# Kernel optimization log

Hardware: AMD Instinct MI355X
Metric: run time of the kernel (lower is better)

The kernel has to match this reference:

```python
import jax, jax.numpy as jnp
import numpy as np

B, H, W, C = 1, 64, 64, 768
NUM_HEADS = 12
HEAD_DIM = C // NUM_HEADS  # 64


def setup_inputs() -> dict:
    key = jax.random.key(0)
    ks = jax.random.split(key, 7)
    s = 0.02
    return {
        "imagelike_bhwc": jax.random.normal(ks[0], (B, H, W, C), dtype=jnp.float32),
        "qkv_w": jax.random.normal(ks[1], (C, 3 * C), dtype=jnp.float32) * s,
        "qkv_b": jax.random.normal(ks[2], (3 * C,), dtype=jnp.float32) * s,
        "proj_w": jax.random.normal(ks[3], (C, C), dtype=jnp.float32) * s,
        "proj_b": jax.random.normal(ks[4], (C,), dtype=jnp.float32) * s,
        "rel_pos_h": jax.random.normal(ks[5], (2 * H - 1, HEAD_DIM), dtype=jnp.float32) * s,
        "rel_pos_w": jax.random.normal(ks[6], (2 * W - 1, HEAD_DIM), dtype=jnp.float32) * s,
    }


def reference(imagelike_bhwc, qkv_w, qkv_b, proj_w, proj_b, rel_pos_h, rel_pos_w):
    b, h, w, c = imagelike_bhwc.shape
    n = h * w
    nh, hd = NUM_HEADS, c // NUM_HEADS
    scale = hd ** (-0.5)

    # qkv projection -> (3, B*nh, N, hd)
    qkv = imagelike_bhwc @ qkv_w + qkv_b  # (b,h,w,3c)
    qkv = qkv.reshape(b, n, 3, nh, hd).transpose(2, 0, 3, 1, 4).reshape(3, b * nh, n, hd)
    q, k, v = qkv[0], qkv[1], qkv[2]

    # scaled dot-product scores
    attn = jnp.einsum("bqd,bkd->bqk", q * scale, k)  # (b*nh, n, n)

    # decomposed relative position bias (query grid == key grid == base grid)
    idx_h = jnp.arange(h)[:, None] - jnp.arange(h)[None, :] + (h - 1)  # (h,h)
    idx_w = jnp.arange(w)[:, None] - jnp.arange(w)[None, :] + (w - 1)  # (w,w)
    Rh = rel_pos_h[idx_h]  # (h, h, hd)
    Rw = rel_pos_w[idx_w]  # (w, w, hd)
    r_q = q.reshape(b * nh, h, w, hd)
    rel_h = jnp.einsum("bhwc,hkc->bhwk", r_q, Rh)  # (b*nh, h, w, h)
    rel_w = jnp.einsum("bhwc,wkc->bhwk", r_q, Rw)  # (b*nh, h, w, w)
    bias = (rel_h[:, :, :, :, None] + rel_w[:, :, :, None, :]).reshape(b * nh, n, n)

    attn = jax.nn.softmax(attn + bias, axis=-1)
    out = jnp.einsum("bqk,bkd->bqd", attn, v)  # (b*nh, n, hd)

    out = out.reshape(b, nh, h, w, hd).transpose(0, 2, 3, 1, 4).reshape(b, h, w, c)
    return out @ proj_w + proj_b
```

## Files before the change

kernel.cpp:

```cpp
#include <hip/hip_runtime.h>
#include <stdint.h>

typedef unsigned short u16;
typedef __bf16 bf16x8 __attribute__((ext_vector_type(8)));
typedef float f32x4 __attribute__((ext_vector_type(4)));
typedef unsigned short ushort8 __attribute__((ext_vector_type(8)));
typedef unsigned short ushort4v __attribute__((ext_vector_type(4)));
typedef uint32_t uint4v __attribute__((ext_vector_type(4)));

#define MFMA __builtin_amdgcn_mfma_f32_16x16x32_bf16
#define EXP2 __builtin_amdgcn_exp2f

__device__ __forceinline__ u16 f2bf(float f){
  uint32_t u = __builtin_bit_cast(uint32_t, f);
  u += 0x7fffu + ((u >> 16) & 1u);
  return (u16)(u >> 16);
}
__device__ __forceinline__ float bf2f(u16 h){
  uint32_t u = ((uint32_t)h) << 16;
  return __builtin_bit_cast(float, u);
}
__device__ __forceinline__ uint32_t cvtpk(float lo, float hi){
  uint32_t r;
  asm("v_cvt_pk_bf16_f32 %0, %1, %2" : "=v"(r) : "v"(lo), "v"(hi));
  return r;
}
__device__ __forceinline__ bf16x8 ld8(const u16* p){
  return __builtin_bit_cast(bf16x8, *(const ushort8*)p);
}
__device__ __forceinline__ void gload16(const void* g, void* l){
  __builtin_amdgcn_global_load_lds((__attribute__((address_space(1))) void*)(void*)g,
                                   (__attribute__((address_space(3))) void*)l, 16, 0, 0);
}


__device__ __forceinline__ void tr_body(const float* __restrict__ in, u16* __restrict__ out,
                                        int R, int Cc, int bx, int by, int t, float* tile ){
  int r0 = bx*64, c0 = by*64;
  int c = t & 63, r4 = t >> 6;
  for (int i = 0; i < 16; ++i)
    tile[(r4 + i*4)*65 + c] = in[(size_t)(r0 + r4 + i*4)*Cc + c0 + c];
  __syncthreads();
  for (int i = 0; i < 16; ++i){
    int rr = r4 + i*4;
    out[(size_t)(c0 + rr)*R + r0 + c] = f2bf(tile[c*65 + rr]);
  }
}

__global__ __launch_bounds__(256) void k_prep(const float* __restrict__ X32,
                                              const float* __restrict__ qkvw,
                                              const float* __restrict__ projw,
                                              const float* __restrict__ rposh,
                                              const float* __restrict__ rposw,
                                              u16* __restrict__ Xb, u16* __restrict__ W1T,
                                              u16* __restrict__ PT,
                                              u16* __restrict__ rh8, u16* __restrict__ rw8){
  __shared__ float tile[64*65];
  const int b = blockIdx.x, t = threadIdx.x;
  if (b < 1536){
    int i = b*256 + t;
    const float4* p = (const float4*)X32;
    float4 a = p[i*2], c = p[i*2+1];
    ushort8 o;
    o[0]=f2bf(a.x); o[1]=f2bf(a.y); o[2]=f2bf(a.z); o[3]=f2bf(a.w);
    o[4]=f2bf(c.x); o[5]=f2bf(c.y); o[6]=f2bf(c.z); o[7]=f2bf(c.w);
    ((ushort8*)Xb)[i] = o;
  } else if (b < 1968){
    int bb = b - 1536;
    tr_body(qkvw, W1T, 768, 2304, bb % 12, bb / 12, t, tile);
  } else if (b < 2112){
    int bb = b - 1968;
    tr_body(projw, PT, 768, 768, bb % 12, bb / 12, t, tile);
  } else {
    int i = (b - 2112)*256 + t;
    if (i < 8192)      rh8[i] = f2bf(i < 8128 ? rposh[i]*8.0f : 0.0f);
    else { int j = i - 8192; rw8[j] = f2bf(j < 8128 ? rposw[j]*8.0f : 0.0f); }
  }
}


__global__ __launch_bounds__(256) void k_qkv(const u16* __restrict__ X, const u16* __restrict__ WT,
                                             const float* __restrict__ bias,
                                             u16* __restrict__ Qs, u16* __restrict__ Kf, u16* __restrict__ Vf){
  __shared__ __align__(16) u16 At[128*64];
  __shared__ __align__(16) u16 Bt[128*64];
  __shared__ __align__(16) u16 Tt[4][64*72];
  const int tid = threadIdx.x, lane = tid & 63, w = tid >> 6;
  const int m0 = blockIdx.x*128, n0 = blockIdx.y*128;
  const int wr = (w >> 1)*64, wc = (w & 1)*64;
  const int lr = lane & 15, lg = lane >> 4;
  const int srcRow = w*32 + (lane >> 3);
  const int srcK   = (lane & 7)*8;
  f32x4 acc[4][4] = {};
  for (int kt = 0; kt < 12; ++kt){
    const int kbase = kt*64;
    for (int s = 0; s < 4; ++s){
      gload16(X  + (size_t)(m0 + srcRow + s*8)*768 + kbase + srcK, At + (w*32 + s*8)*64);
      gload16(WT + (size_t)(n0 + srcRow + s*8)*768 + kbase + srcK, Bt + (w*32 + s*8)*64);
    }
    __syncthreads();
    bf16x8 af[2][4], bfr[2][4];
    for (int ks = 0; ks < 2; ++ks)
      for (int i = 0; i < 4; ++i){
        af[ks][i]  = ld8(At + (wr + i*16 + lr)*64 + ks*32 + lg*8);
        bfr[ks][i] = ld8(Bt + (wc + i*16 + lr)*64 + ks*32 + lg*8);
      }
    for (int ks = 0; ks < 2; ++ks)
      for (int mi = 0; mi < 4; ++mi)
        for (int ni = 0; ni < 4; ++ni)
          acc[mi][ni] = MFMA(af[ks][mi], bfr[ks][ni], acc[mi][ni], 0, 0, 0);
    __syncthreads();
  }
  const int colbase = n0 + wc;
  const int s3 = colbase / 768;
  const int hh = (colbase % 768) >> 6;
  const int rowbase = m0 + wr;
  if (s3 == 0){
    for (int mi = 0; mi < 4; ++mi)
      for (int ni = 0; ni < 4; ++ni){
        float bv = bias[colbase + ni*16 + lr];
        for (int r = 0; r < 4; ++r){
          int row = rowbase + mi*16 + lg*4 + r;
          Qs[((size_t)hh*4096 + row)*64 + ni*16 + lr] =
              f2bf((acc[mi][ni][r] + bv)*(0.125f*1.44269504f));
        }
      }
  } else {
    u16* T = Tt[w];
    for (int mi = 0; mi < 4; ++mi)
      for (int ni = 0; ni < 4; ++ni){
        float bv = bias[colbase + ni*16 + lr];
        for (int r = 0; r < 4; ++r){
          int row_l = mi*16 + lg*4 + r, col_l = ni*16 + lr;
          u16 v = f2bf(acc[mi][ni][r] + bv);
          if (s3 == 1) T[row_l*72 + col_l] = v;
          else         T[col_l*72 + row_l] = v;
        }
      }
    const int kb = rowbase >> 6;
    u16* dst = (s3 == 1 ? Kf : Vf) + ((size_t)hh*64 + kb)*4096 + lane*8;
    if (s3 == 1){
      #pragma unroll
      for (int f = 0; f < 8; ++f){
        int a = f >> 1, ks = f & 1;
        *(ushort8*)&dst[f*512] = *(const ushort8*)&T[(a*16 + lr)*72 + ks*32 + lg*8];
      }
    } else {
      #pragma unroll
      for (int f = 0; f < 8; ++f){
        int a = f >> 1, ks = f & 1;
        const int rowb = (a*16 + lr)*72 + ks*32 + lg*4;
        ushort4v lo = *(const ushort4v*)&T[rowb];
        ushort4v hi = *(const ushort4v*)&T[rowb + 16];
        ushort8 o;
        o[0]=lo[0]; o[1]=lo[1]; o[2]=lo[2]; o[3]=lo[3];
        o[4]=hi[0]; o[5]=hi[1]; o[6]=hi[2]; o[7]=hi[3];
        *(ushort8*)&dst[f*512] = o;
      }
    }
  }
}


__global__ __launch_bounds__(256) void k_rel(const u16* __restrict__ Qs, const u16* __restrict__ Rh8,
                                             const u16* __restrict__ Rw8,
                                             u16* __restrict__ relh, u16* __restrict__ relw){
  __shared__ __align__(16) u16 Ql[64*64];
  __shared__ __align__(16) u16 Rhl[64*64];
  __shared__ __align__(16) u16 Rwl[128*64];
  const int tid = threadIdx.x, lane = tid & 63, w = tid >> 6;
  const int qh = blockIdx.x, h = blockIdx.y;
  const int lr = lane & 15, lg = lane >> 4;
  for (int j = 0; j < 2; ++j){
    int ch = tid + 256*j;
    int row = ch >> 3, k8 = (ch & 7)*8;
    *(ushort8*)&Ql[row*64 + k8]  = *(const ushort8*)&Qs[((size_t)h*4096 + qh*64 + row)*64 + k8];
    *(ushort8*)&Rhl[row*64 + k8] = *(const ushort8*)&Rh8[(qh + row)*64 + k8];
  }
  for (int j = 0; j < 4; ++j){
    int ch = tid + 256*j;
    int row = ch >> 3, k8 = (ch & 7)*8;
    *(ushort8*)&Rwl[row*64 + k8] = *(const ushort8*)&Rw8[row*64 + k8];
  }
  __syncthreads();
  bf16x8 a[2];
  for (int ks = 0; ks < 2; ++ks) a[ks] = ld8(Ql + (w*16 + lr)*64 + ks*32 + lg*8);
  for (int ct = 0; ct < 4; ++ct){
    f32x4 c = {};
    for (int ks = 0; ks < 2; ++ks)
      c = MFMA(a[ks], ld8(Rhl + (ct*16 + lr)*64 + ks*32 + lg*8), c, 0, 0, 0);
    int kh = 63 - (ct*16 + lr);
    for (int r = 0; r < 4; ++r){
      int qw = w*16 + lg*4 + r;
      relh[((size_t)h*4096 + qh*64 + qw)*64 + kh] = f2bf(c[r]);
    }
  }
  for (int ct = 0; ct < 8; ++ct){
    f32x4 c = {};
    for (int ks = 0; ks < 2; ++ks)
      c = MFMA(a[ks], ld8(Rwl + (ct*16 + lr)*64 + ks*32 + lg*8), c, 0, 0, 0);
    int cc = ct*16 + lr;
    for (int r = 0; r < 4; ++r){
      int qw = w*16 + lg*4 + r;
      int kw = qw + 63 - cc;
      if (kw >= 0 && kw < 64)
        relw[((size_t)h*4096 + qh*64 + qw)*64 + kw] = f2bf(c[r]);
    }
  }
}


__global__ __launch_bounds__(256, 3) void k_flash(const u16* __restrict__ Qs, const u16* __restrict__ Kf,
                                                  const u16* __restrict__ Vf,
                                                  const u16* __restrict__ relh, const u16* __restrict__ relw,
                                                  u16* __restrict__ Ob){
  __shared__ __align__(16) u16 Kl[2][4096];
  __shared__ __align__(16) u16 Vl[2][4096];
  const int tid = threadIdx.x, lane = tid & 63, w = tid >> 6;
  const int b = blockIdx.x;
  const int p = (b & 7)*96 + (b >> 3);
  const int h = p >> 6, qb = p & 63;
  const int lr = lane & 15, lg = lane >> 4;
  const size_t hq = (size_t)h*4096;
  const int q = qb*64 + w*16 + lr;

  const bf16x8 qf0 = ld8(Qs + (hq + q)*64 + lg*8);
  const bf16x8 qf1 = ld8(Qs + (hq + q)*64 + 32 + lg*8);
  float rwf[4][4];
  #pragma unroll
  for (int ct = 0; ct < 4; ++ct){
    ushort4v t = *(const ushort4v*)&relw[(hq + q)*64 + ct*16 + lg*4];
    #pragma unroll
    for (int r = 0; r < 4; ++r) rwf[ct][r] = bf2f(t[r]);
  }

  const u16* KfH = Kf + (size_t)h*262144;
  const u16* VfH = Vf + (size_t)h*262144;
  const u16* rhbase = relh + (hq + q)*64;

  float m = -1e30f, lsum = 0.f;
  f32x4 oacc[4] = {};

  auto stage = [&](int buf, int kb){
    const u16* ks = KfH + kb*4096 + w*1024 + lane*8;
    const u16* vs = VfH + kb*4096 + w*1024 + lane*8;
    gload16(ks,       &Kl[buf][w*1024]);
    gload16(ks + 512, &Kl[buf][w*1024 + 512]);
    gload16(vs,       &Vl[buf][w*1024]);
    gload16(vs + 512, &Vl[buf][w*1024 + 512]);
  };

#define ITERBODY(KB, BUF)                                                     \
  {                                                                           \
    const u16* KL = Kl[BUF] + lane*8;                                         \
    const u16* VL = Vl[BUF] + lane*8;                                         \
    const float rhv = bf2f(rhbase[KB]);                                       \
    f32x4 s[4];                                                               \
    _Pragma("unroll")                                                         \
    for (int ct = 0; ct < 4; ++ct){                                           \
      _Pragma("unroll")                                                       \
      for (int r = 0; r < 4; ++r) s[ct][r] = rhv + rwf[ct][r];                \
    }                                                                         \
    __builtin_amdgcn_s_setprio(1);                                            \
    _Pragma("unroll")                                                         \
    for (int ct = 0; ct < 4; ++ct){                                           \
      s[ct] = MFMA(ld8(KL + (ct*2)*512),   qf0, s[ct], 0, 0, 0);              \
      s[ct] = MFMA(ld8(KL + (ct*2+1)*512), qf1, s[ct], 0, 0, 0);              \
    }                                                                         \
    __builtin_amdgcn_s_setprio(0);                                            \
                                       \
    float pm0 = fmaxf(fmaxf(s[0][0], s[0][1]), fmaxf(fmaxf(s[0][2], s[0][3]), \
                      fmaxf(s[1][0], s[1][1])));                              \
    float pm1 = fmaxf(fmaxf(s[1][2], s[1][3]), fmaxf(fmaxf(s[2][0], s[2][1]), \
                      fmaxf(s[2][2], s[2][3])));                              \
    float pm2 = fmaxf(fmaxf(s[3][0], s[3][1]), fmaxf(s[3][2], s[3][3]));      \
    float pm = fmaxf(fmaxf(pm0, pm1), pm2);                                   \
             \
    if (__any(pm > m)){                                                       \
      pm = fmaxf(pm, __shfl_xor(pm, 16, 64));                                 \
      pm = fmaxf(pm, __shfl_xor(pm, 32, 64));                                 \
      const float nm = fmaxf(m, pm);                                          \
      const float corr = EXP2(m - nm);                                        \
      m = nm;                                                                 \
      lsum *= corr;                                                           \
      _Pragma("unroll")                                                       \
      for (int dt = 0; dt < 4; ++dt)                                          \
        _Pragma("unroll")                                                     \
        for (int r = 0; r < 4; ++r) oacc[dt][r] *= corr;                      \
    }                                                                         \
    float rs = 0.f;                                                           \
    _Pragma("unroll")                                                         \
    for (int ct = 0; ct < 4; ++ct){                                           \
      _Pragma("unroll")                                                       \
      for (int r = 0; r < 4; ++r){                                            \
        float p2 = EXP2(s[ct][r] - m);                                        \
        s[ct][r] = p2; rs += p2;                                              \
      }                                                                       \
    }                                                                         \
    lsum += rs;                           \
             \
    uint4v u0, u1;                                                            \
    u0[0] = cvtpk(s[0][0], s[0][1]); u0[1] = cvtpk(s[0][2], s[0][3]);         \
    u0[2] = cvtpk(s[1][0], s[1][1]); u0[3] = cvtpk(s[1][2], s[1][3]);         \
    u1[0] = cvtpk(s[2][0], s[2][1]); u1[1] = cvtpk(s[2][2], s[2][3]);         \
    u1[2] = cvtpk(s[3][0], s[3][1]); u1[3] = cvtpk(s[3][2], s[3][3]);         \
    bf16x8 pa0 = __builtin_bit_cast(bf16x8, u0);                              \
    bf16x8 pa1 = __builtin_bit_cast(bf16x8, u1);                              \
    __builtin_amdgcn_s_setprio(1);                                            \
    _Pragma("unroll")                                                         \
    for (int dt = 0; dt < 4; ++dt){                                           \
      oacc[dt] = MFMA(ld8(VL + (dt*2)*512),   pa0, oacc[dt], 0, 0, 0);        \
      oacc[dt] = MFMA(ld8(VL + (dt*2+1)*512), pa1, oacc[dt], 0, 0, 0);        \
    }                                                                         \
    __builtin_amdgcn_s_setprio(0);                                            \
  }

  stage(0, 0);
  __syncthreads();
  for (int kb2 = 0; kb2 < 64; kb2 += 2){
    stage(1, (kb2 + 1) & 63);
    ITERBODY(kb2, 0)
    __syncthreads();
    stage(0, (kb2 + 2) & 63);
    ITERBODY(kb2 + 1, 1)
    __syncthreads();
  }
#undef ITERBODY

  lsum += __shfl_xor(lsum, 16, 64);
  lsum += __shfl_xor(lsum, 32, 64);
  const float inv = 1.0f / lsum;
  #pragma unroll
  for (int dt = 0; dt < 4; ++dt){
    ushort4v pk;
    #pragma unroll
    for (int r = 0; r < 4; ++r) pk[r] = f2bf(oacc[dt][r]*inv);
    *(ushort4v*)&Ob[(size_t)q*768 + h*64 + dt*16 + lg*4] = pk;
  }
}


__global__ __launch_bounds__(256) void k_proj(const u16* __restrict__ A, const u16* __restrict__ WT,
                                              const float* __restrict__ bias, float* __restrict__ out){
  __shared__ __align__(16) u16 At[128*64];
  __shared__ __align__(16) u16 Bt[128*64];
  const int tid = threadIdx.x, lane = tid & 63, w = tid >> 6;
  const int m0 = blockIdx.x*128, n0 = blockIdx.y*128;
  const int wr = (w >> 1)*64, wc = (w & 1)*64;
  const int lr = lane & 15, lg = lane >> 4;
  const int srcRow = w*32 + (lane >> 3);
  const int srcK   = (lane & 7)*8;
  f32x4 acc[4][4] = {};
  for (int kt = 0; kt < 12; ++kt){
    const int kbase = kt*64;
    for (int s = 0; s < 4; ++s){
      gload16(A  + (size_t)(m0 + srcRow + s*8)*768 + kbase + srcK, At + (w*32 + s*8)*64);
      gload16(WT + (size_t)(n0 + srcRow + s*8)*768 + kbase + srcK, Bt + (w*32 + s*8)*64);
    }
    __syncthreads();
    bf16x8 af[2][4], bfr[2][4];
    for (int ks = 0; ks < 2; ++ks)
      for (int i = 0; i < 4; ++i){
        af[ks][i]  = ld8(At + (wr + i*16 + lr)*64 + ks*32 + lg*8);
        bfr[ks][i] = ld8(Bt + (wc + i*16 + lr)*64 + ks*32 + lg*8);
      }
    for (int ks = 0; ks < 2; ++ks)
      for (int mi = 0; mi < 4; ++mi)
        for (int ni = 0; ni < 4; ++ni)
          acc[mi][ni] = MFMA(af[ks][mi], bfr[ks][ni], acc[mi][ni], 0, 0, 0);
    __syncthreads();
  }
  for (int mi = 0; mi < 4; ++mi)
    for (int ni = 0; ni < 4; ++ni){
      int col = n0 + wc + ni*16 + lr;
      float bv = bias[col];
      for (int r = 0; r < 4; ++r){
        int row = m0 + wr + mi*16 + lg*4 + r;
        out[(size_t)row*768 + col] = acc[mi][ni][r] + bv;
      }
    }
}


extern "C" void kernel_launch(void* const* d_in, const int* in_sizes, int n_in,
                              void* d_out, int out_size, void* d_ws, size_t ws_size,
                              hipStream_t stream){
  const float* X32   = (const float*)d_in[0];
  const float* qkvw  = (const float*)d_in[1];
  const float* qkvb  = (const float*)d_in[2];
  const float* projw = (const float*)d_in[3];
  const float* projb = (const float*)d_in[4];
  const float* rposh = (const float*)d_in[5];
  const float* rposw = (const float*)d_in[6];

  u16* Xb  = (u16*)d_ws;
  u16* W1T = Xb  + 3145728;
  u16* PT  = W1T + 1769472;
  u16* Rh8 = PT  + 589824;
  u16* Rw8 = Rh8 + 8192;
  u16* Qs  = Rw8 + 8192;
  u16* Kf  = Qs  + 3145728;
  u16* Vf  = Kf  + 3145728;
  u16* Rlh = Vf  + 3145728;
  u16* Rlw = Rlh + 3145728;
  u16* Ob  = Rlw + 3145728;
  float* out = (float*)d_out;

  k_prep <<<2176, 256, 0, stream>>>(X32, qkvw, projw, rposh, rposw, Xb, W1T, PT, Rh8, Rw8);
  k_qkv  <<<dim3(32, 18), 256, 0, stream>>>(Xb, W1T, qkvb, Qs, Kf, Vf);
  k_rel  <<<dim3(64, 12), 256, 0, stream>>>(Qs, Rh8, Rw8, Rlh, Rlw);
  k_flash<<<768, 256, 0, stream>>>(Qs, Kf, Vf, Rlh, Rlw, Ob);
  k_proj <<<dim3(32, 6), 256, 0, stream>>>(Ob, PT, projb, out);
}
```

Before: 162.0 us.

## Fuse relative-position bias computation into flash attention kernel

Removes the separate k_rel kernel and computes the rel_h and rel_w bias terms inside k_flash's prologue via MFMA against Rh8/Rw8, holding them in per-wave shared memory. This removes one launch plus the write and re-read of two large bias tensors in global memory. In exchange the flash kernel gains extra prologue work and shared memory, which may lower occupancy. The first K/V stage is issued before the prologue so that load overlaps the bias compute.

```diff
diff --git a/kernel.cpp b/kernel.cpp
--- a/kernel.cpp
+++ b/kernel.cpp
@@ -162,60 +162,14 @@
 }
 
 
-__global__ __launch_bounds__(256) void k_rel(const u16* __restrict__ Qs, const u16* __restrict__ Rh8,
-                                             const u16* __restrict__ Rw8,
-                                             u16* __restrict__ relh, u16* __restrict__ relw){
-  __shared__ __align__(16) u16 Ql[64*64];
-  __shared__ __align__(16) u16 Rhl[64*64];
-  __shared__ __align__(16) u16 Rwl[128*64];
-  const int tid = threadIdx.x, lane = tid & 63, w = tid >> 6;
-  const int qh = blockIdx.x, h = blockIdx.y;
-  const int lr = lane & 15, lg = lane >> 4;
-  for (int j = 0; j < 2; ++j){
-    int ch = tid + 256*j;
-    int row = ch >> 3, k8 = (ch & 7)*8;
-    *(ushort8*)&Ql[row*64 + k8]  = *(const ushort8*)&Qs[((size_t)h*4096 + qh*64 + row)*64 + k8];
-    *(ushort8*)&Rhl[row*64 + k8] = *(const ushort8*)&Rh8[(qh + row)*64 + k8];
-  }
-  for (int j = 0; j < 4; ++j){
-    int ch = tid + 256*j;
-    int row = ch >> 3, k8 = (ch & 7)*8;
-    *(ushort8*)&Rwl[row*64 + k8] = *(const ushort8*)&Rw8[row*64 + k8];
-  }
-  __syncthreads();
-  bf16x8 a[2];
-  for (int ks = 0; ks < 2; ++ks) a[ks] = ld8(Ql + (w*16 + lr)*64 + ks*32 + lg*8);
-  for (int ct = 0; ct < 4; ++ct){
-    f32x4 c = {};
-    for (int ks = 0; ks < 2; ++ks)
-      c = MFMA(a[ks], ld8(Rhl + (ct*16 + lr)*64 + ks*32 + lg*8), c, 0, 0, 0);
-    int kh = 63 - (ct*16 + lr);
-    for (int r = 0; r < 4; ++r){
-      int qw = w*16 + lg*4 + r;
-      relh[((size_t)h*4096 + qh*64 + qw)*64 + kh] = f2bf(c[r]);
-    }
-  }
-  for (int ct = 0; ct < 8; ++ct){
-    f32x4 c = {};
-    for (int ks = 0; ks < 2; ++ks)
-      c = MFMA(a[ks], ld8(Rwl + (ct*16 + lr)*64 + ks*32 + lg*8), c, 0, 0, 0);
-    int cc = ct*16 + lr;
-    for (int r = 0; r < 4; ++r){
-      int qw = w*16 + lg*4 + r;
-      int kw = qw + 63 - cc;
-      if (kw >= 0 && kw < 64)
-        relw[((size_t)h*4096 + qh*64 + qw)*64 + kw] = f2bf(c[r]);
-    }
-  }
-}
-
-
 __global__ __launch_bounds__(256, 3) void k_flash(const u16* __restrict__ Qs, const u16* __restrict__ Kf,
                                                   const u16* __restrict__ Vf,
-                                                  const u16* __restrict__ relh, const u16* __restrict__ relw,
+                                                  const u16* __restrict__ Rh8, const u16* __restrict__ Rw8,
                                                   u16* __restrict__ Ob){
   __shared__ __align__(16) u16 Kl[2][4096];
   __shared__ __align__(16) u16 Vl[2][4096];
+  __shared__ __align__(16) u16 RhL[4][16*68];
+  __shared__ __align__(16) u16 RwL[4][16*68];
   const int tid = threadIdx.x, lane = tid & 63, w = tid >> 6;
   const int b = blockIdx.x;
   const int p = (b & 7)*96 + (b >> 3);
@@ -224,22 +178,8 @@
   const size_t hq = (size_t)h*4096;
   const int q = qb*64 + w*16 + lr;
 
-  const bf16x8 qf0 = ld8(Qs + (hq + q)*64 + lg*8);
-  const bf16x8 qf1 = ld8(Qs + (hq + q)*64 + 32 + lg*8);
-  float rwf[4][4];
-  #pragma unroll
-  for (int ct = 0; ct < 4; ++ct){
-    ushort4v t = *(const ushort4v*)&relw[(hq + q)*64 + ct*16 + lg*4];
-    #pragma unroll
-    for (int r = 0; r < 4; ++r) rwf[ct][r] = bf2f(t[r]);
-  }
-
   const u16* KfH = Kf + (size_t)h*262144;
   const u16* VfH = Vf + (size_t)h*262144;
-  const u16* rhbase = relh + (hq + q)*64;
-
-  float m = -1e30f, lsum = 0.f;
-  f32x4 oacc[4] = {};
 
   auto stage = [&](int buf, int kb){
     const u16* ks = KfH + kb*4096 + w*1024 + lane*8;
@@ -250,11 +190,51 @@
     gload16(vs + 512, &Vl[buf][w*1024 + 512]);
   };
 
+  stage(0, 0);
+
+  const bf16x8 qf0 = ld8(Qs + (hq + q)*64 + lg*8);
+  const bf16x8 qf1 = ld8(Qs + (hq + q)*64 + 32 + lg*8);
+
+  u16* RhLw = RhL[w];
+  #pragma unroll
+  for (int ct = 0; ct < 4; ++ct){
+    f32x4 c = {};
+    const u16* r0 = Rh8 + (qb + 63 - (ct*16 + lr))*64 + lg*8;
+    c = MFMA(ld8(r0),      qf0, c, 0, 0, 0);
+    c = MFMA(ld8(r0 + 32), qf1, c, 0, 0, 0);
+    #pragma unroll
+    for (int r = 0; r < 4; ++r)
+      RhLw[lr*68 + ct*16 + lg*4 + r] = f2bf(c[r]);
+  }
+  u16* RwLw = RwL[w];
+  #pragma unroll
+  for (int ct2 = 0; ct2 < 8; ++ct2){
+    f32x4 c = {};
+    const u16* r0 = Rw8 + (ct2*16 + lr)*64 + lg*8;
+    c = MFMA(ld8(r0),      qf0, c, 0, 0, 0);
+    c = MFMA(ld8(r0 + 32), qf1, c, 0, 0, 0);
+    #pragma unroll
+    for (int r = 0; r < 4; ++r){
+      int kw = (w*16 + lr) + 63 - (ct2*16 + lg*4 + r);
+      if (kw >= 0 && kw < 64) RwLw[lr*68 + kw] = f2bf(c[r]);
+    }
+  }
+  float rwf[4][4];
+  #pragma unroll
+  for (int ct = 0; ct < 4; ++ct){
+    ushort4v t = *(const ushort4v*)&RwLw[lr*68 + ct*16 + lg*4];
+    #pragma unroll
+    for (int r = 0; r < 4; ++r) rwf[ct][r] = bf2f(t[r]);
+  }
+
+  float m = -1e30f, lsum = 0.f;
+  f32x4 oacc[4] = {};
+
 #define ITERBODY(KB, BUF)                                                     \
   {                                                                           \
     const u16* KL = Kl[BUF] + lane*8;                                         \
     const u16* VL = Vl[BUF] + lane*8;                                         \
-    const float rhv = bf2f(rhbase[KB]);                                       \
+    const float rhv = bf2f(RhLw[lr*68 + (KB)]);                               \
     f32x4 s[4];                                                               \
     _Pragma("unroll")                                                         \
     for (int ct = 0; ct < 4; ++ct){                                           \
@@ -315,7 +295,6 @@
     __builtin_amdgcn_s_setprio(0);                                            \
   }
 
-  stage(0, 0);
   __syncthreads();
   for (int kb2 = 0; kb2 < 64; kb2 += 2){
     stage(1, (kb2 + 1) & 63);
@@ -401,14 +380,11 @@
   u16* Qs  = Rw8 + 8192;
   u16* Kf  = Qs  + 3145728;
   u16* Vf  = Kf  + 3145728;
-  u16* Rlh = Vf  + 3145728;
-  u16* Rlw = Rlh + 3145728;
-  u16* Ob  = Rlw + 3145728;
+  u16* Ob  = Vf  + 3145728;
   float* out = (float*)d_out;
 
   k_prep <<<2176, 256, 0, stream>>>(X32, qkvw, projw, rposh, rposw, Xb, W1T, PT, Rh8, Rw8);
   k_qkv  <<<dim3(32, 18), 256, 0, stream>>>(Xb, W1T, qkvb, Qs, Kf, Vf);
-  k_rel  <<<dim3(64, 12), 256, 0, stream>>>(Qs, Rh8, Rw8, Rlh, Rlw);
-  k_flash<<<768, 256, 0, stream>>>(Qs, Kf, Vf, Rlh, Rlw, Ob);
+  k_flash<<<768, 256, 0, stream>>>(Qs, Kf, Vf, Rh8, Rw8, Ob);
   k_proj <<<dim3(32, 6), 256, 0, stream>>>(Ob, PT, projb, out);
 }
```

Measured after the change: 156.4 us. -3.4%, faster.
